# Optimization experiments

Measured on AMD Instinct MI355X. Metric: run time of the kernel, lower is better.

Reference implementation:

```python
import jax, jax.numpy as jnp
import numpy as np

B, T, D, H = 32, 2048, 256, 256


def setup_inputs() -> dict:
    key = jax.random.key(0)
    ks = jax.random.split(key, 7)
    s = 1.0 / np.sqrt(H)  # PyTorch GRUCell default init scale
    x = jax.random.normal(ks[0], (B, T, D), jnp.float32)
    seg = jax.random.randint(ks[1], (B, T), 0, 2, jnp.int32)  # 1 = continue segment, 0 = boundary (write+reset)
    lengths = jax.random.randint(ks[2], (B,), T // 2, T, jnp.int32)
    W_ih = jax.random.uniform(ks[3], (3 * H, D), jnp.float32, -s, s)
    W_hh = jax.random.uniform(ks[4], (3 * H, H), jnp.float32, -s, s)
    b_ih = jax.random.uniform(ks[5], (3 * H,), jnp.float32, -s, s)
    b_hh = jax.random.uniform(ks[6], (3 * H,), jnp.float32, -s, s)
    return {"x": x, "seg": seg, "lengths": lengths,
            "W_ih": W_ih, "W_hh": W_hh, "b_ih": b_ih, "b_hh": b_hh}


def gru_cell(xt, h, W_ih, W_hh, b_ih, b_hh):
    # PyTorch GRUCell math
    gi = xt @ W_ih.T + b_ih          # [B, 3H]
    gh = h @ W_hh.T + b_hh           # [B, 3H]
    i_r, i_z, i_n = jnp.split(gi, 3, axis=-1)
    h_r, h_z, h_n = jnp.split(gh, 3, axis=-1)
    r = jax.nn.sigmoid(i_r + h_r)
    z = jax.nn.sigmoid(i_z + h_z)
    n = jnp.tanh(i_n + r * h_n)
    return (1.0 - z) * n + z * h


def reference(x, seg, lengths, W_ih, W_hh, b_ih, b_hh):
    Bn, Tn, _ = x.shape
    Hn = W_hh.shape[1]
    barange = jnp.arange(Bn)

    def step(carry, inp):
        h, idx, out = carry
        xt, seg_t, t = inp
        h_new = gru_cell(xt, h, W_ih, W_hh, b_ih, b_hh)
        # write h at per-example position idx where segment boundary and t < length
        write = (seg_t == 0) & (t < lengths)                     # [B] bool
        cur = out[barange, idx]                                  # [B, H]
        out = out.at[barange, idx].set(jnp.where(write[:, None], h_new, cur))
        idx = idx + write.astype(idx.dtype)
        # reset hidden to zero at segment boundaries (seg==0)
        h = seg_t.astype(h_new.dtype)[:, None] * h_new
        return (h, idx, out), None

    h0 = jnp.zeros((Bn, Hn), x.dtype)
    idx0 = jnp.zeros((Bn,), jnp.int32)
    # static max output length = Tn (original uses data-dependent max; we pad to T)
    out0 = jnp.zeros((Bn, Tn, Hn), x.dtype)
    (h, idx, out), _ = jax.lax.scan(
        step, (h0, idx0, out0),
        (jnp.transpose(x, (1, 0, 2)), seg.T, jnp.arange(Tn)))
    return out, idx
```

## Files before the change

### kernel.cpp

```cpp
#include <hip/hip_runtime.h>
#include <cstdint>
#include <cstddef>

#define TT 2048
#define BB 32
#define DD 256
#define HH 256

using bf16x8 = __attribute__((ext_vector_type(8))) short;
using f32x4  = __attribute__((ext_vector_type(4))) float;

static const size_t REC_OFF  = 64;
static const size_t REC2_OFF = REC_OFF  + (size_t)32768 * 16;
static const size_t BF_OFF   = REC2_OFF + (size_t)32768 * 16;

__device__ __forceinline__ uint16_t f2bf(float v) {
    unsigned int u = __float_as_uint(v);
    u += 0x7FFF + ((u >> 16) & 1);
    return (uint16_t)(u >> 16);
}
__device__ __forceinline__ float bf2f(uint16_t h) {
    return __uint_as_float(((unsigned int)h) << 16);
}
__device__ __forceinline__ float sigmoidf_(float v) {
    return 1.f / (1.f + __expf(-v));
}
__device__ __forceinline__ float tanhf_(float v) {
    v = fminf(fmaxf(v, -30.f), 30.f);
    float e = __expf(-2.f * v);
    return (1.f - e) / (1.f + e);
}

__global__ void k_prep(const float* __restrict__ Wih, const float* __restrict__ Whh,
                       uint16_t* __restrict__ BF) {
    int i = blockIdx.x * 256 + threadIdx.x;
    if (i >= 768 * 64) return;
    int lane = i & 63, f = i >> 6;
    int kk = f & 7, t = f >> 3;
    int g = t % 6, wct = t / 6;
    int w = wct >> 1, ct = wct & 1;
    int col = w * 32 + ct * 16 + (lane & 15);
    int k0 = kk * 32 + ((lane >> 4) << 3);
    const float* W = (g < 3) ? Wih : Whh;
    const float* src = W + (size_t)((g % 3) * 256 + col) * DD + k0;
    bf16x8 v;
    #pragma unroll
    for (int e = 0; e < 8; ++e) v[e] = (short)f2bf(src[e]);
    *(bf16x8*)&BF[(size_t)f * 512 + lane * 8] = v;
}

__global__ void k_meta(const int* __restrict__ seg, const int* __restrict__ lengths,
                       int4* __restrict__ recs, int* __restrict__ counters,
                       float* __restrict__ outIdx) {
    int b = blockIdx.x;
    int tid = threadIdx.x;
    int len = lengths[b];
    const int* s = seg + (size_t)b * TT;
    const int CH = TT / 256;
    int t0 = tid * CH;

    int cnt = 0;
    for (int t = t0; t < t0 + CH; ++t)
        cnt += (s[t] == 0 && t < len) ? 1 : 0;

    __shared__ int part[256];
    __shared__ int base;
    part[tid] = cnt;
    __syncthreads();
    if (tid == 0) {
        int run = 0;
        for (int i = 0; i < 256; ++i) { int v = part[i]; part[i] = run; run += v; }
        base = atomicAdd(&counters[0], run);
        outIdx[b] = (float)run;
    }
    __syncthreads();

    int run = part[tid];
    for (int t = t0; t < t0 + CH; ++t) {
        if (s[t] == 0 && t < len) {
            int ss = t - 1;
            while (ss >= 0 && s[ss] != 0) --ss;
            int slot = base + run;
            if (slot < 32768) recs[slot] = make_int4(b, ss + 1, t, run);
            ++run;
        }
    }
}

__global__ void k_sort(const int4* __restrict__ recs, int4* __restrict__ recs2,
                       const int* __restrict__ counters) {
    __shared__ int hist[64];
    __shared__ int off[64];
    int n = counters[0]; if (n > 32768) n = 32768;
    int tid = threadIdx.x;
    if (tid < 64) hist[tid] = 0;
    __syncthreads();
    for (int i = tid; i < n; i += 1024) {
        int4 r = recs[i];
        int len = r.z - r.y + 1;
        atomicAdd(&hist[min(len, 63)], 1);
    }
    __syncthreads();
    if (tid == 0) {
        int run = 0;
        for (int b = 63; b >= 0; --b) { off[b] = run; run += hist[b]; }
    }
    __syncthreads();
    if (tid < 64) hist[tid] = 0;
    __syncthreads();
    for (int i = tid; i < n; i += 1024) {
        int4 r = recs[i];
        int len = r.z - r.y + 1;
        int b = min(len, 63);
        int pos = off[b] + atomicAdd(&hist[b], 1);
        recs2[pos] = r;
    }
}

__global__ __launch_bounds__(512, 2) void k_main(
    const float* __restrict__ x, const uint16_t* __restrict__ BF,
    const float* __restrict__ b_ih, const float* __restrict__ b_hh,
    const int4* __restrict__ recs, int* __restrict__ counters,
    float* __restrict__ out)
{
    extern __shared__ uint16_t smem[];
    uint16_t* xH = smem;
    uint16_t* xL = smem + 16384;
    uint16_t* hH = smem + 32768;
    uint16_t* hL = smem + 49152;
    __shared__ int rb[64], rt[64], re[64], rp[64], alive[64];
    __shared__ int liveRTS[4];
    __shared__ int anyAliveS, nsegS;

    const int tid  = threadIdx.x;
    const int lane = tid & 63;
    const int w    = tid >> 6;
    const int lcol = lane & 15;
    const int lk   = lane >> 4;

    for (int i = tid; i < 16384; i += 512) { hH[i] = 0; hL[i] = 0; }
    if (tid < 64) alive[tid] = 0;
    if (tid == 0) nsegS = min(counters[0], 32768);
    __syncthreads();
    const int nseg = nsegS;

    float bR[2], bZ[2], bIN[2], bHN[2];
    #pragma unroll
    for (int ct = 0; ct < 2; ++ct) {
        int c = w * 32 + ct * 16 + lcol;
        bR[ct]  = b_ih[c]       + b_hh[c];
        bZ[ct]  = b_ih[256 + c] + b_hh[256 + c];
        bIN[ct] = b_ih[512 + c];
        bHN[ct] = b_hh[512 + c];
    }
    const uint16_t* BFw = BF + (size_t)w * 96 * 512;

    for (;;) {
        if (tid < 64) {
            int m = tid;
            int al = alive[m];
            if (al) { if (rt[m] >= re[m]) al = 0; else rt[m] = rt[m] + 1; }
            unsigned long long deadm = __ballot(!al);
            int base = 0;
            if (tid == 0 && deadm) base = atomicAdd(&counters[1], __popcll(deadm));
            base = __shfl(base, 0);
            if (!al) {
                int rank = __popcll(deadm & ((1ULL << tid) - 1));
                int sidx = base + rank;
                if (sidx < nseg) {
                    int4 r = recs[sidx];
                    rb[m] = r.x; rt[m] = r.y; re[m] = r.z; rp[m] = r.w;
                    al = 1;
                }
            }
            alive[m] = al;
            unsigned long long am = __ballot(al);
            if (tid == 0) anyAliveS = (am != 0ULL) ? 1 : 0;
            if (tid < 4) liveRTS[tid] = (int)((am >> (tid * 16)) & 0xFFFFULL);
        }
        __syncthreads();
        if (!anyAliveS) break;

        {
            int row = tid >> 3, j = tid & 7;
            if (alive[row]) {
                const float* xp = x + ((size_t)rb[row] * TT + rt[row]) * DD + j * 32;
                #pragma unroll
                for (int u = 0; u < 4; ++u) {
                    float4 a = *(const float4*)(xp + u * 8);
                    float4 b = *(const float4*)(xp + u * 8 + 4);
                    float vv[8] = {a.x, a.y, a.z, a.w, b.x, b.y, b.z, b.w};
                    bf16x8 vh, vl;
                    #pragma unroll
                    for (int e = 0; e < 8; ++e) {
                        uint16_t hi = f2bf(vv[e]);
                        vh[e] = (short)hi;
                        vl[e] = (short)f2bf(vv[e] - bf2f(hi));
                    }
                    int cs = j * 4 + u;
                    int o = row * 256 + ((cs ^ (row & 15)) << 3);
                    *(bf16x8*)&xH[o] = vh;
                    *(bf16x8*)&xL[o] = vl;
                }
            }
        }
        __syncthreads();

        int lv0 = liveRTS[0], lv1 = liveRTS[1], lv2 = liveRTS[2], lv3 = liveRTS[3];
        int lv[4] = {lv0, lv1, lv2, lv3};

        f32x4 acc[4][4][2];
        #pragma unroll
        for (int rtI = 0; rtI < 4; ++rtI)
            #pragma unroll
            for (int g = 0; g < 4; ++g)
                #pragma unroll
                for (int ct = 0; ct < 2; ++ct)
                    acc[rtI][g][ct] = (f32x4){0.f, 0.f, 0.f, 0.f};

        for (int kk = 0; kk < 8; ++kk) {
            bf16x8 ax[4][2], ah[4][2];
            int cs = kk * 4 + lk;
            #pragma unroll
            for (int rtI = 0; rtI < 4; ++rtI) if (lv[rtI]) {
                int row = rtI * 16 + lcol;
                int o = row * 256 + ((cs ^ (row & 15)) << 3);
                ax[rtI][0] = *(const bf16x8*)&xH[o];
                ax[rtI][1] = *(const bf16x8*)&xL[o];
                ah[rtI][0] = *(const bf16x8*)&hH[o];
                ah[rtI][1] = *(const bf16x8*)&hL[o];
            }
            #pragma unroll
            for (int g = 0; g < 6; ++g) {
                const int ai = (g == 0 || g == 3) ? 0 : (g == 1 || g == 4) ? 1 : (g == 2) ? 2 : 3;
                #pragma unroll
                for (int ct = 0; ct < 2; ++ct) {
                    bf16x8 B = *(const bf16x8*)&BFw[((ct * 48 + g * 8 + kk) << 9) + (lane << 3)];
                    #pragma unroll
                    for (int rtI = 0; rtI < 4; ++rtI) if (lv[rtI]) {
                        if (g < 3) {
                            acc[rtI][ai][ct] = __builtin_amdgcn_mfma_f32_16x16x32_bf16(ax[rtI][0], B, acc[rtI][ai][ct], 0, 0, 0);
                            acc[rtI][ai][ct] = __builtin_amdgcn_mfma_f32_16x16x32_bf16(ax[rtI][1], B, acc[rtI][ai][ct], 0, 0, 0);
                        } else {
                            acc[rtI][ai][ct] = __builtin_amdgcn_mfma_f32_16x16x32_bf16(ah[rtI][0], B, acc[rtI][ai][ct], 0, 0, 0);
                            acc[rtI][ai][ct] = __builtin_amdgcn_mfma_f32_16x16x32_bf16(ah[rtI][1], B, acc[rtI][ai][ct], 0, 0, 0);
                        }
                    }
                }
            }
        }
        __syncthreads();

        #pragma unroll
        for (int rtI = 0; rtI < 4; ++rtI) if (lv[rtI]) {
            #pragma unroll
            for (int q = 0; q < 4; ++q) {
                int row = rtI * 16 + lk * 4 + q;
                if (!alive[row]) continue;
                int em = (rt[row] == re[row]);
                #pragma unroll
                for (int ct = 0; ct < 2; ++ct) {
                    int c = w * 32 + ct * 16 + lcol;
                    float gr  = acc[rtI][0][ct][q] + bR[ct];
                    float gz  = acc[rtI][1][ct][q] + bZ[ct];
                    float gin = acc[rtI][2][ct][q] + bIN[ct];
                    float ghn = acc[rtI][3][ct][q] + bHN[ct];
                    float rr = sigmoidf_(gr);
                    float zz = sigmoidf_(gz);
                    float nn = tanhf_(gin + rr * ghn);
                    int o = row * 256 + (((c >> 3) ^ (row & 15)) << 3) + (c & 7);
                    float hold = bf2f(hH[o]) + bf2f(hL[o]);
                    float hnew = (1.f - zz) * nn + zz * hold;
                    if (em) {
                        out[((size_t)rb[row] * TT + rp[row]) * HH + c] = hnew;
                        hnew = 0.f;
                    }
                    uint16_t hi = f2bf(hnew);
                    hH[o] = hi;
                    hL[o] = f2bf(hnew - bf2f(hi));
                }
            }
        }
        __syncthreads();
    }
}

extern "C" void kernel_launch(void* const* d_in, const int* in_sizes, int n_in,
                              void* d_out, int out_size, void* d_ws, size_t ws_size,
                              hipStream_t stream) {
    const float* x   = (const float*)d_in[0];
    const int*   seg = (const int*)d_in[1];
    const int*   len = (const int*)d_in[2];
    const float* Wih = (const float*)d_in[3];
    const float* Whh = (const float*)d_in[4];
    const float* bih = (const float*)d_in[5];
    const float* bhh = (const float*)d_in[6];
    float* out = (float*)d_out;

    int*      counters = (int*)d_ws;
    int4*     recs     = (int4*)((char*)d_ws + REC_OFF);
    int4*     recs2    = (int4*)((char*)d_ws + REC2_OFF);
    uint16_t* BF       = (uint16_t*)((char*)d_ws + BF_OFF);

    static int lds_set = 0;
    if (!lds_set) {
        hipFuncSetAttribute(reinterpret_cast<const void*>(&k_main),
                            hipFuncAttributeMaxDynamicSharedMemorySize, 131072);
        lds_set = 1;
    }

    hipMemsetAsync(d_out, 0, (size_t)out_size * sizeof(float), stream);
    hipMemsetAsync(d_ws, 0, 64, stream);

    k_prep<<<192, 256, 0, stream>>>(Wih, Whh, BF);
    k_meta<<<BB, 256, 0, stream>>>(seg, len, recs, counters, out + (size_t)BB * TT * HH);
    k_sort<<<1, 1024, 0, stream>>>(recs, recs2, counters);
    k_main<<<256, 512, 131072, stream>>>(x, BF, bih, bhh, recs2, counters, out);
}
```

Before: 781.6 us.

## Halve per-block segment slots to 32 and double blocks for higher occupancy

Each block of k_main now processes 32 concurrent segments instead of 64. That halves LDS use to 64 KB and the accumulator registers to two row tiles. The grid grows to 512 blocks, launch bounds rise to 4 blocks per CU, and the x-gate and h-gate MFMA loops are split so the h fragments load later, which cuts live registers. The aim is more concurrent waves and better latency hiding on the sequential per-step loop, at the cost of loading each weight fragment once per 32 rows instead of once per 64, so weight reuse drops.

```diff
diff --git a/kernel.cpp b/kernel.cpp
--- a/kernel.cpp
+++ b/kernel.cpp
@@ -117,7 +117,7 @@
     }
 }
 
-__global__ __launch_bounds__(512, 2) void k_main(
+__global__ __launch_bounds__(512, 4) void k_main(
     const float* __restrict__ x, const uint16_t* __restrict__ BF,
     const float* __restrict__ b_ih, const float* __restrict__ b_hh,
     const int4* __restrict__ recs, int* __restrict__ counters,
@@ -125,11 +125,11 @@
 {
     extern __shared__ uint16_t smem[];
     uint16_t* xH = smem;
-    uint16_t* xL = smem + 16384;
-    uint16_t* hH = smem + 32768;
-    uint16_t* hL = smem + 49152;
-    __shared__ int rb[64], rt[64], re[64], rp[64], alive[64];
-    __shared__ int liveRTS[4];
+    uint16_t* xL = smem + 8192;
+    uint16_t* hH = smem + 16384;
+    uint16_t* hL = smem + 24576;
+    __shared__ int rb[32], rt[32], re[32], rp[32], alive[32];
+    __shared__ int liveRTS[2];
     __shared__ int anyAliveS, nsegS;
 
     const int tid  = threadIdx.x;
@@ -138,8 +138,8 @@
     const int lcol = lane & 15;
     const int lk   = lane >> 4;
 
-    for (int i = tid; i < 16384; i += 512) { hH[i] = 0; hL[i] = 0; }
-    if (tid < 64) alive[tid] = 0;
+    for (int i = tid; i < 8192; i += 512) { hH[i] = 0; hL[i] = 0; }
+    if (tid < 32) alive[tid] = 0;
     if (tid == 0) nsegS = min(counters[0], 32768);
     __syncthreads();
     const int nseg = nsegS;
@@ -156,7 +156,7 @@
     const uint16_t* BFw = BF + (size_t)w * 96 * 512;
 
     for (;;) {
-        if (tid < 64) {
+        if (tid < 32) {
             int m = tid;
             int al = alive[m];
             if (al) { if (rt[m] >= re[m]) al = 0; else rt[m] = rt[m] + 1; }
@@ -176,17 +176,17 @@
             alive[m] = al;
             unsigned long long am = __ballot(al);
             if (tid == 0) anyAliveS = (am != 0ULL) ? 1 : 0;
-            if (tid < 4) liveRTS[tid] = (int)((am >> (tid * 16)) & 0xFFFFULL);
+            if (tid < 2) liveRTS[tid] = (int)((am >> (tid * 16)) & 0xFFFFULL);
         }
         __syncthreads();
         if (!anyAliveS) break;
 
         {
-            int row = tid >> 3, j = tid & 7;
+            int row = tid >> 4, j = tid & 15;
             if (alive[row]) {
-                const float* xp = x + ((size_t)rb[row] * TT + rt[row]) * DD + j * 32;
-                #pragma unroll
-                for (int u = 0; u < 4; ++u) {
+                const float* xp = x + ((size_t)rb[row] * TT + rt[row]) * DD + j * 16;
+                #pragma unroll
+                for (int u = 0; u < 2; ++u) {
                     float4 a = *(const float4*)(xp + u * 8);
                     float4 b = *(const float4*)(xp + u * 8 + 4);
                     float vv[8] = {a.x, a.y, a.z, a.w, b.x, b.y, b.z, b.w};
@@ -197,7 +197,7 @@
                         vh[e] = (short)hi;
                         vl[e] = (short)f2bf(vv[e] - bf2f(hi));
                     }
-                    int cs = j * 4 + u;
+                    int cs = j * 2 + u;
                     int o = row * 256 + ((cs ^ (row & 15)) << 3);
                     *(bf16x8*)&xH[o] = vh;
                     *(bf16x8*)&xL[o] = vl;
@@ -206,12 +206,11 @@
         }
         __syncthreads();
 
-        int lv0 = liveRTS[0], lv1 = liveRTS[1], lv2 = liveRTS[2], lv3 = liveRTS[3];
-        int lv[4] = {lv0, lv1, lv2, lv3};
-
-        f32x4 acc[4][4][2];
+        const int lv0 = liveRTS[0], lv1 = liveRTS[1];
+
+        f32x4 acc[2][4][2];
         #pragma unroll
-        for (int rtI = 0; rtI < 4; ++rtI)
+        for (int rtI = 0; rtI < 2; ++rtI)
             #pragma unroll
             for (int g = 0; g < 4; ++g)
                 #pragma unroll
@@ -219,32 +218,44 @@
                     acc[rtI][g][ct] = (f32x4){0.f, 0.f, 0.f, 0.f};
 
         for (int kk = 0; kk < 8; ++kk) {
-            bf16x8 ax[4][2], ah[4][2];
-            int cs = kk * 4 + lk;
+            const int cs = kk * 4 + lk;
+            const int o0 = lcol * 256        + ((cs ^ lcol) << 3);
+            const int o1 = (16 + lcol) * 256 + ((cs ^ lcol) << 3);
+
+            bf16x8 ax0h, ax0l, ax1h, ax1l;
+            if (lv0) { ax0h = *(const bf16x8*)&xH[o0]; ax0l = *(const bf16x8*)&xL[o0]; }
+            if (lv1) { ax1h = *(const bf16x8*)&xH[o1]; ax1l = *(const bf16x8*)&xL[o1]; }
             #pragma unroll
-            for (int rtI = 0; rtI < 4; ++rtI) if (lv[rtI]) {
-                int row = rtI * 16 + lcol;
-                int o = row * 256 + ((cs ^ (row & 15)) << 3);
-                ax[rtI][0] = *(const bf16x8*)&xH[o];
-                ax[rtI][1] = *(const bf16x8*)&xL[o];
-                ah[rtI][0] = *(const bf16x8*)&hH[o];
-                ah[rtI][1] = *(const bf16x8*)&hL[o];
-            }
-            #pragma unroll
-            for (int g = 0; g < 6; ++g) {
-                const int ai = (g == 0 || g == 3) ? 0 : (g == 1 || g == 4) ? 1 : (g == 2) ? 2 : 3;
+            for (int g = 0; g < 3; ++g) {
                 #pragma unroll
                 for (int ct = 0; ct < 2; ++ct) {
                     bf16x8 B = *(const bf16x8*)&BFw[((ct * 48 + g * 8 + kk) << 9) + (lane << 3)];
-                    #pragma unroll
-                    for (int rtI = 0; rtI < 4; ++rtI) if (lv[rtI]) {
-                        if (g < 3) {
-                            acc[rtI][ai][ct] = __builtin_amdgcn_mfma_f32_16x16x32_bf16(ax[rtI][0], B, acc[rtI][ai][ct], 0, 0, 0);
-                            acc[rtI][ai][ct] = __builtin_amdgcn_mfma_f32_16x16x32_bf16(ax[rtI][1], B, acc[rtI][ai][ct], 0, 0, 0);
-                        } else {
-                            acc[rtI][ai][ct] = __builtin_amdgcn_mfma_f32_16x16x32_bf16(ah[rtI][0], B, acc[rtI][ai][ct], 0, 0, 0);
-                            acc[rtI][ai][ct] = __builtin_amdgcn_mfma_f32_16x16x32_bf16(ah[rtI][1], B, acc[rtI][ai][ct], 0, 0, 0);
-                        }
+                    if (lv0) {
+                        acc[0][g][ct] = __builtin_amdgcn_mfma_f32_16x16x32_bf16(ax0h, B, acc[0][g][ct], 0, 0, 0);
+                        acc[0][g][ct] = __builtin_amdgcn_mfma_f32_16x16x32_bf16(ax0l, B, acc[0][g][ct], 0, 0, 0);
+                    }
+                    if (lv1) {
+                        acc[1][g][ct] = __builtin_amdgcn_mfma_f32_16x16x32_bf16(ax1h, B, acc[1][g][ct], 0, 0, 0);
+                        acc[1][g][ct] = __builtin_amdgcn_mfma_f32_16x16x32_bf16(ax1l, B, acc[1][g][ct], 0, 0, 0);
+                    }
+                }
+            }
+            bf16x8 ah0h, ah0l, ah1h, ah1l;
+            if (lv0) { ah0h = *(const bf16x8*)&hH[o0]; ah0l = *(const bf16x8*)&hL[o0]; }
+            if (lv1) { ah1h = *(const bf16x8*)&hH[o1]; ah1l = *(const bf16x8*)&hL[o1]; }
+            #pragma unroll
+            for (int g = 0; g < 3; ++g) {
+                const int ai = (g == 2) ? 3 : g;
+                #pragma unroll
+                for (int ct = 0; ct < 2; ++ct) {
+                    bf16x8 B = *(const bf16x8*)&BFw[((ct * 48 + (g + 3) * 8 + kk) << 9) + (lane << 3)];
+                    if (lv0) {
+                        acc[0][ai][ct] = __builtin_amdgcn_mfma_f32_16x16x32_bf16(ah0h, B, acc[0][ai][ct], 0, 0, 0);
+                        acc[0][ai][ct] = __builtin_amdgcn_mfma_f32_16x16x32_bf16(ah0l, B, acc[0][ai][ct], 0, 0, 0);
+                    }
+                    if (lv1) {
+                        acc[1][ai][ct] = __builtin_amdgcn_mfma_f32_16x16x32_bf16(ah1h, B, acc[1][ai][ct], 0, 0, 0);
+                        acc[1][ai][ct] = __builtin_amdgcn_mfma_f32_16x16x32_bf16(ah1l, B, acc[1][ai][ct], 0, 0, 0);
                     }
                 }
             }
@@ -252,7 +263,8 @@
         __syncthreads();
 
         #pragma unroll
-        for (int rtI = 0; rtI < 4; ++rtI) if (lv[rtI]) {
+        for (int rtI = 0; rtI < 2; ++rtI) {
+            if (!(rtI ? lv1 : lv0)) continue;
             #pragma unroll
             for (int q = 0; q < 4; ++q) {
                 int row = rtI * 16 + lk * 4 + q;
@@ -305,7 +317,7 @@
     static int lds_set = 0;
     if (!lds_set) {
         hipFuncSetAttribute(reinterpret_cast<const void*>(&k_main),
-                            hipFuncAttributeMaxDynamicSharedMemorySize, 131072);
+                            hipFuncAttributeMaxDynamicSharedMemorySize, 65536);
         lds_set = 1;
     }
 
@@ -315,5 +327,5 @@
     k_prep<<<192, 256, 0, stream>>>(Wih, Whh, BF);
     k_meta<<<BB, 256, 0, stream>>>(seg, len, recs, counters, out + (size_t)BB * TT * HH);
     k_sort<<<1, 1024, 0, stream>>>(recs, recs2, counters);
-    k_main<<<256, 512, 131072, stream>>>(x, BF, bih, bhh, recs2, counters, out);
-}
+    k_main<<<512, 512, 65536, stream>>>(x, BF, bih, bhh, recs2, counters, out);
+}
```

After: 908.5 us. 1.16x slower.
